# Kernel tuning notes

Measured on AMD Instinct MI355X. Metric: run time of the kernel, lower is better.

## Reference

```python
import jax, jax.numpy as jnp
import numpy as np

MAX_ATOMS = 80
MAX_DEGREE = 4
MAX_RINGS = 10
RING_SIZE = 8
BATCH = 16384


def setup_inputs() -> dict:
    key = jax.random.key(0)
    k1, k2 = jax.random.split(key)
    # neighbor indices in [-1, MAX_ATOMS); -1 == null neighbor slot
    edges = jax.random.randint(k1, (BATCH, MAX_ATOMS, MAX_DEGREE), -1, MAX_ATOMS).astype(jnp.float32)
    # ring member atom indices in [-1, MAX_ATOMS); -1 == padding
    rings = jax.random.randint(k2, (BATCH, MAX_RINGS, RING_SIZE), -1, MAX_ATOMS).astype(jnp.int32)
    return {"edges": edges, "rings": rings}


def reference(edges, rings):
    # edges: [B, A, D] float (cast to int, -1 = null); rings: [B, R, S] int
    e = edges.astype(jnp.int32)
    B, A, D = e.shape
    R = rings.shape[1]
    # membership[b, r, a] = atom a appears in ring r of molecule b  -> [B, R, A]
    membership = jnp.any(rings[:, :, :, None] == jnp.arange(A, dtype=jnp.int32), axis=2)
    # gather neighbor membership: nbr_mem[b, r, a, d] = membership[b, r, e[b, a, d]]
    e_clip = jnp.clip(e, 0, A - 1)  # safe index for null (-1) slots, masked below
    idx = jnp.broadcast_to(e_clip.reshape(B, 1, A * D), (B, R, A * D))
    nbr_mem = jnp.take_along_axis(membership, idx, axis=2).reshape(B, R, A, D)
    # bond (a, d) is a ring bond iff some ring contains both a and its neighbor,
    # and the neighbor slot is not null
    in_ring = jnp.any(membership[:, :, :, None] & nbr_mem, axis=1)  # [B, A, D]
    valid = e != -1
    out = (in_ring & valid).astype(jnp.float32)
    return out.reshape(B, A, D, 1)
```

## Files before the change

### kernel.cpp

```cpp
#include <hip/hip_runtime.h>

#define MAX_ATOMS   80
#define MAX_DEGREE  4
#define MAX_RINGS   10
#define RING_SIZE   8
#define RING_FLAT   (MAX_RINGS * RING_SIZE)
#define EDGE_FLAT   (MAX_ATOMS * MAX_DEGREE)
#define MOLS_PER_BLOCK 4

__device__ __forceinline__ float bond_val(int nb, unsigned ma, const unsigned* m) {
    int c = nb < 0 ? 0 : (nb > MAX_ATOMS - 1 ? MAX_ATOMS - 1 : nb);
    return ((nb >= 0) && (ma & m[c])) ? 1.0f : 0.0f;
}

__global__ __launch_bounds__(256) void Find_Ring_Bonds_kernel(
    const float* __restrict__ edges,
    const int*   __restrict__ rings,
    float*       __restrict__ out,
    int B)
{
    __shared__ unsigned mtab[MOLS_PER_BLOCK][MAX_ATOMS];

    const int wave = threadIdx.x >> 6;
    const int lane = threadIdx.x & 63;
    const int mol  = blockIdx.x * MOLS_PER_BLOCK + wave;
    if (mol >= B) return;

    unsigned* m = mtab[wave];

    const float4* e4 = (const float4*)(edges + (size_t)mol * EDGE_FLAT);
    float4*       o4 = (float4*)(out   + (size_t)mol * EDGE_FLAT);

    int4 ra = {0,0,0,0}, rb = {0,0,0,0};
    const bool ringlane = (lane < MAX_RINGS);
    if (ringlane) {
        const int4* rp = (const int4*)(rings + (size_t)mol * RING_FLAT + lane * RING_SIZE);
        ra = rp[0];
        rb = rp[1];
    }

    const bool hi = (lane < MAX_ATOMS - 64);
    float4 ev0 = e4[lane];
    float4 ev1;
    if (hi) ev1 = e4[64 + lane];

    unsigned w0 = 0u, w1 = 0u, w2 = 0u;
    if (ringlane) {
        int vs[8] = {ra.x, ra.y, ra.z, ra.w, rb.x, rb.y, rb.z, rb.w};
        #pragma unroll
        for (int s = 0; s < 8; ++s) {
            int v = vs[s];
            unsigned b = 1u << (v & 31);
            w0 |= (v >= 0 && v < 32) ? b : 0u;
            w1 |= (v >= 32 && v < 64) ? b : 0u;
            w2 |= (v >= 64)           ? b : 0u;
        }
    }

    unsigned m0 = 0u, m1 = 0u;
    #pragma unroll
    for (int r = 0; r < MAX_RINGS; ++r) {
        unsigned rw0 = (unsigned)__builtin_amdgcn_readlane((int)w0, r);
        unsigned rw1 = (unsigned)__builtin_amdgcn_readlane((int)w1, r);
        unsigned rw2 = (unsigned)__builtin_amdgcn_readlane((int)w2, r);
        unsigned long long lo64 = ((unsigned long long)rw1 << 32) | (unsigned long long)rw0;
        m0 |= ((unsigned)(lo64 >> lane) & 1u) << r;
        m1 |= ((rw2 >> lane) & 1u) << r;
    }

    m[lane] = m0;
    if (hi) m[64 + lane] = m1;

    {
        float4 r;
        r.x = bond_val((int)ev0.x, m0, m);
        r.y = bond_val((int)ev0.y, m0, m);
        r.z = bond_val((int)ev0.z, m0, m);
        r.w = bond_val((int)ev0.w, m0, m);
        o4[lane] = r;
    }
    if (hi) {
        float4 r;
        r.x = bond_val((int)ev1.x, m1, m);
        r.y = bond_val((int)ev1.y, m1, m);
        r.z = bond_val((int)ev1.z, m1, m);
        r.w = bond_val((int)ev1.w, m1, m);
        o4[64 + lane] = r;
    }
}

extern "C" void kernel_launch(void* const* d_in, const int* in_sizes, int n_in,
                              void* d_out, int out_size, void* d_ws, size_t ws_size,
                              hipStream_t stream) {
    const float* edges = (const float*)d_in[0];
    const int*   rings = (const int*)d_in[1];
    float*       out   = (float*)d_out;

    const int B = in_sizes[0] / EDGE_FLAT;
    const int grid = (B + MOLS_PER_BLOCK - 1) / MOLS_PER_BLOCK;

    Find_Ring_Bonds_kernel<<<grid, 256, 0, stream>>>(edges, rings, out, B);
}
```

Measured before the change: 76.87 us.

## Process two molecules per wave and build ring membership via LDS atomicOr

Each wave now handles two molecules, so all 64 lanes help with loads and every lane of the 160-atom span is used. Ring membership is built by having lanes scatter bits into shared memory with atomicOr, replacing the register readlane transpose. This adds two block-wide barriers, LDS atomics and zero-initialisation, and halves the number of blocks in the grid.

```diff
diff --git a/kernel.cpp b/kernel.cpp
--- a/kernel.cpp
+++ b/kernel.cpp
@@ -6,11 +6,13 @@
 #define RING_SIZE   8
 #define RING_FLAT   (MAX_RINGS * RING_SIZE)
 #define EDGE_FLAT   (MAX_ATOMS * MAX_DEGREE)
-#define MOLS_PER_BLOCK 4
+#define WAVES_PER_BLOCK 4
+#define MOLS_PER_WAVE   2
+#define MOLS_PER_BLOCK  (WAVES_PER_BLOCK * MOLS_PER_WAVE)
 
-__device__ __forceinline__ float bond_val(int nb, unsigned ma, const unsigned* m) {
+__device__ __forceinline__ float bond_val(int nb, unsigned ma, const unsigned* mt) {
     int c = nb < 0 ? 0 : (nb > MAX_ATOMS - 1 ? MAX_ATOMS - 1 : nb);
-    return ((nb >= 0) && (ma & m[c])) ? 1.0f : 0.0f;
+    return ((nb >= 0) && (ma & mt[c])) ? 1.0f : 0.0f;
 }
 
 __global__ __launch_bounds__(256) void Find_Ring_Bonds_kernel(
@@ -19,73 +21,82 @@
     float*       __restrict__ out,
     int B)
 {
-    __shared__ unsigned mtab[MOLS_PER_BLOCK][MAX_ATOMS];
+    __shared__ unsigned mtab[WAVES_PER_BLOCK][2 * MAX_ATOMS];
 
     const int wave = threadIdx.x >> 6;
     const int lane = threadIdx.x & 63;
-    const int mol  = blockIdx.x * MOLS_PER_BLOCK + wave;
-    if (mol >= B) return;
+    const int pm   = (blockIdx.x * WAVES_PER_BLOCK + wave) * MOLS_PER_WAVE;
+    const bool live = (pm < B);
+    const int nmol  = !live ? 0 : ((pm + 1 < B) ? 2 : 1);
+    const int limit = nmol * MAX_ATOMS;
 
     unsigned* m = mtab[wave];
 
-    const float4* e4 = (const float4*)(edges + (size_t)mol * EDGE_FLAT);
-    float4*       o4 = (float4*)(out   + (size_t)mol * EDGE_FLAT);
+    const float4* e4 = (const float4*)(edges + (size_t)pm * EDGE_FLAT);
+    float4*       o4 = (float4*)(out   + (size_t)pm * EDGE_FLAT);
 
-    int4 ra = {0,0,0,0}, rb = {0,0,0,0};
-    const bool ringlane = (lane < MAX_RINGS);
-    if (ringlane) {
-        const int4* rp = (const int4*)(rings + (size_t)mol * RING_FLAT + lane * RING_SIZE);
-        ra = rp[0];
-        rb = rp[1];
+    int4 rv = {-1, -1, -1, -1};
+    const bool rl = lane < (limit >> 2);
+    if (rl) rv = ((const int4*)(rings + (size_t)pm * RING_FLAT))[lane];
+
+    const bool v0 = lane < limit;
+    const bool v1 = (64 + lane) < limit;
+    const bool v2 = (lane < 32) && ((128 + lane) < limit);
+    float4 ev0, ev1, ev2;
+    if (v0) ev0 = e4[lane];
+    if (v1) ev1 = e4[64 + lane];
+    if (v2) ev2 = e4[128 + lane];
+
+    if (live) {
+        m[lane]      = 0u;
+        m[64 + lane] = 0u;
+        if (lane < 32) m[128 + lane] = 0u;
     }
+    __syncthreads();
 
-    const bool hi = (lane < MAX_ATOMS - 64);
-    float4 ev0 = e4[lane];
-    float4 ev1;
-    if (hi) ev1 = e4[64 + lane];
-
-    unsigned w0 = 0u, w1 = 0u, w2 = 0u;
-    if (ringlane) {
-        int vs[8] = {ra.x, ra.y, ra.z, ra.w, rb.x, rb.y, rb.z, rb.w};
+    if (rl) {
+        const int e0 = lane * 4;
+        const int vs[4] = {rv.x, rv.y, rv.z, rv.w};
         #pragma unroll
-        for (int s = 0; s < 8; ++s) {
-            int v = vs[s];
-            unsigned b = 1u << (v & 31);
-            w0 |= (v >= 0 && v < 32) ? b : 0u;
-            w1 |= (v >= 32 && v < 64) ? b : 0u;
-            w2 |= (v >= 64)           ? b : 0u;
+        for (int j = 0; j < 4; ++j) {
+            const int ej   = e0 + j;
+            const int moff = (ej >= MAX_ATOMS) ? MAX_ATOMS : 0;
+            const unsigned bit = 1u << ((ej - moff) >> 3);
+            const int v = vs[j];
+            if (v >= 0) atomicOr(&m[moff + v], bit);
         }
     }
+    __syncthreads();
 
-    unsigned m0 = 0u, m1 = 0u;
-    #pragma unroll
-    for (int r = 0; r < MAX_RINGS; ++r) {
-        unsigned rw0 = (unsigned)__builtin_amdgcn_readlane((int)w0, r);
-        unsigned rw1 = (unsigned)__builtin_amdgcn_readlane((int)w1, r);
-        unsigned rw2 = (unsigned)__builtin_amdgcn_readlane((int)w2, r);
-        unsigned long long lo64 = ((unsigned long long)rw1 << 32) | (unsigned long long)rw0;
-        m0 |= ((unsigned)(lo64 >> lane) & 1u) << r;
-        m1 |= ((rw2 >> lane) & 1u) << r;
-    }
-
-    m[lane] = m0;
-    if (hi) m[64 + lane] = m1;
-
-    {
+    if (v0) {
+        const unsigned ma = m[lane];
         float4 r;
-        r.x = bond_val((int)ev0.x, m0, m);
-        r.y = bond_val((int)ev0.y, m0, m);
-        r.z = bond_val((int)ev0.z, m0, m);
-        r.w = bond_val((int)ev0.w, m0, m);
+        r.x = bond_val((int)ev0.x, ma, m);
+        r.y = bond_val((int)ev0.y, ma, m);
+        r.z = bond_val((int)ev0.z, ma, m);
+        r.w = bond_val((int)ev0.w, ma, m);
         o4[lane] = r;
     }
-    if (hi) {
+    if (v1) {
+        const int f = 64 + lane;
+        const int moff = (f >= MAX_ATOMS) ? MAX_ATOMS : 0;
+        const unsigned ma = m[f];
         float4 r;
-        r.x = bond_val((int)ev1.x, m1, m);
-        r.y = bond_val((int)ev1.y, m1, m);
-        r.z = bond_val((int)ev1.z, m1, m);
-        r.w = bond_val((int)ev1.w, m1, m);
-        o4[64 + lane] = r;
+        r.x = bond_val((int)ev1.x, ma, m + moff);
+        r.y = bond_val((int)ev1.y, ma, m + moff);
+        r.z = bond_val((int)ev1.z, ma, m + moff);
+        r.w = bond_val((int)ev1.w, ma, m + moff);
+        o4[f] = r;
+    }
+    if (v2) {
+        const int f = 128 + lane;
+        const unsigned ma = m[f];
+        float4 r;
+        r.x = bond_val((int)ev2.x, ma, m + MAX_ATOMS);
+        r.y = bond_val((int)ev2.y, ma, m + MAX_ATOMS);
+        r.z = bond_val((int)ev2.z, ma, m + MAX_ATOMS);
+        r.w = bond_val((int)ev2.w, ma, m + MAX_ATOMS);
+        o4[f] = r;
     }
 }
 
```

Measured after the change: 76.56 us. About the same (-0.4%).
